# Optimization experiments

Hardware: AMD Instinct MI355X
Metric: run time of the kernel (lower is better)

## Reference

```python
import jax, jax.numpy as jnp
import numpy as np


def sage_pool(feat_src, edge_src, edge_dst, num_dst, W_pool, b_pool, W_self, W_neigh, bias):
    """DGL SAGEConv 'pool' aggregator on a bipartite block.
    feat_src: [N_src, in]; first num_dst rows are the dst nodes.
    """
    # per-src-node pool MLP, then gather per edge and scatter-max per dst
    m = jax.nn.relu(feat_src @ W_pool + b_pool)            # [N_src, in]
    agg = jax.ops.segment_max(m[edge_src], edge_dst, num_segments=num_dst)
    agg = jnp.where(jnp.isfinite(agg), agg, jnp.zeros((), agg.dtype))  # DGL: zero for 0-degree
    h_self = feat_src[:num_dst]
    return h_self @ W_self + agg @ W_neigh + bias          # [num_dst, out]


def setup_inputs() -> dict:
    key = jax.random.key(0)
    ks = jax.random.split(key, 16)
    F = 128                      # feat_dim_sum
    N0, N1, N2 = 409600, 40960, 4096
    E0, E1 = 409600, 40960
    inp = {
        "h_item": jax.random.normal(ks[0], (N0, F), jnp.float32),
        "h_item_dst": jax.random.normal(ks[1], (N2, F), jnp.float32),
        "edge_src0": jax.random.randint(ks[2], (E0,), 0, N0),
        "edge_dst0": jax.random.randint(ks[3], (E0,), 0, N1),
        "edge_src1": jax.random.randint(ks[4], (E1,), 0, N1),
        "edge_dst1": jax.random.randint(ks[5], (E1,), 0, N2),
        "num_mid": N1,
    }
    def lin(k, fan_in, fan_out):
        return jax.random.normal(k, (fan_in, fan_out), jnp.float32) / np.sqrt(fan_in)
    # layer 0: SAGEConv(128, 256, 'pool'); layer 1: SAGEConv(256, 128, 'pool')
    inp.update({
        "W_pool0": lin(ks[6], F, F),
        "b_pool0": jnp.zeros((F,), jnp.float32),
        "W_self0": lin(ks[7], F, 2 * F),
        "W_neigh0": lin(ks[8], F, 2 * F),
        "bias0": jnp.zeros((2 * F,), jnp.float32),
        "W_pool1": lin(ks[9], 2 * F, 2 * F),
        "b_pool1": jnp.zeros((2 * F,), jnp.float32),
        "W_self1": lin(ks[10], 2 * F, F),
        "W_neigh1": lin(ks[11], 2 * F, F),
        "bias1": jnp.zeros((F,), jnp.float32),
    })
    return inp


def reference(h_item, h_item_dst, edge_src0, edge_dst0, edge_src1, edge_dst1, num_mid,
              W_pool0, b_pool0, W_self0, W_neigh0, bias0,
              W_pool1, b_pool1, W_self1, W_neigh1, bias1):
    num_dst_final = h_item_dst.shape[0]
    h = sage_pool(h_item, edge_src0, edge_dst0, num_mid,
                  W_pool0, b_pool0, W_self0, W_neigh0, bias0)   # [N1, 2F]
    h = jax.nn.relu(h)  # dropout(0.2) is identity in eval mode
    h = sage_pool(h, edge_src1, edge_dst1, num_dst_final,
                  W_pool1, b_pool1, W_self1, W_neigh1, bias1)   # [N2, F]
    return h_item_dst + h
```

## Files before the change

### kernel.cpp

```cpp
#include <hip/hip_runtime.h>
#include <hip/hip_bf16.h>
#include <cstdint>


typedef unsigned int uint32;
typedef unsigned short ushort_t;

typedef __attribute__((ext_vector_type(8))) short short8v;
typedef __attribute__((ext_vector_type(4))) float float4v;

__device__ __forceinline__ float bf_to_f(unsigned short u) {
    union { uint32 u; float f; } cv; cv.u = ((uint32)u) << 16; return cv.f;
}
__device__ __forceinline__ unsigned short f_to_bf(float f) {
    union { float f; uint32 u; } cv; cv.f = f;
    uint32 u = cv.u;
    uint32 r = (u + 0x7FFFu + ((u >> 16) & 1u)) >> 16;
    return (unsigned short)r;
}

__device__ __forceinline__ int wave_incl_scan(int v) {
    #pragma unroll
    for (int s = 1; s < 64; s <<= 1) {
        int t = __shfl_up(v, s, 64);
        if ((int)(threadIdx.x & 63) >= s) v += t;
    }
    return v;
}

template<int KT, bool ABF>
__device__ __forceinline__ void gemm_seg(
    const void* __restrict__ Av, const ushort_t* __restrict__ Wp, int N,
    int row0, int col0, int tid, int wr, int wc, int l15, int g,
    ushort_t* lds, float4v (&acc)[4][4])
{
    constexpr int ldl = KT + 8;
    __syncthreads();
    if constexpr (ABF) {
        const ushort_t* A = (const ushort_t*)Av;
        constexpr int C8 = KT / 8;
        constexpr int TOT = 128 * C8;
        #pragma unroll 4
        for (int L = tid; L < TOT; L += 256) {
            int row = L / C8;
            int c8  = (L % C8) * 8;
            *(uint4*)&lds[row * ldl + c8] =
                *(const uint4*)(A + (size_t)(row0 + row) * KT + c8);
        }
    } else {
        const float* A = (const float*)Av;
        constexpr int C4 = KT / 4;
        constexpr int TOT = 128 * C4;
        #pragma unroll 4
        for (int L = tid; L < TOT; L += 256) {
            int row = L / C4;
            int c4  = (L % C4) * 4;
            float4 v = *(const float4*)(A + (size_t)(row0 + row) * KT + c4);
            ushort4 pk = make_ushort4(f_to_bf(v.x), f_to_bf(v.y), f_to_bf(v.z), f_to_bf(v.w));
            *(ushort4*)&lds[row * ldl + c4] = pk;
        }
    }
    __syncthreads();

    #pragma unroll
    for (int s = 0; s < KT / 32; ++s) {
        const int kb = s * 4 + g;
        short8v bfr[4], afr[4];
        #pragma unroll
        for (int ni = 0; ni < 4; ++ni) {
            int col = col0 + wc * 64 + ni * 16 + l15;
            bfr[ni] = *(const short8v*)(Wp + ((size_t)kb * N + col) * 8);
        }
        #pragma unroll
        for (int mi = 0; mi < 4; ++mi) {
            int row = wr * 64 + mi * 16 + l15;
            afr[mi] = *(const short8v*)&lds[row * ldl + s * 32 + g * 8];
        }
        #pragma unroll
        for (int mi = 0; mi < 4; ++mi)
            #pragma unroll
            for (int ni = 0; ni < 4; ++ni)
                acc[mi][ni] = __builtin_amdgcn_mfma_f32_16x16x32_bf16(
                    afr[mi], bfr[ni], acc[mi][ni], 0, 0, 0);
    }
}

template<bool RELU, bool BF16_OUT, bool HAS_ADD, int K0T, int K1T, bool A0BF, bool A1BF, int MINW>
__global__ __launch_bounds__(256, MINW) void gemm_mfma(
    const void* __restrict__ A0, const ushort_t* __restrict__ Wp0,
    const void* __restrict__ A1, const ushort_t* __restrict__ Wp1,
    const float* __restrict__ bias, const float* __restrict__ addsrc,
    void* __restrict__ Cout, int N)
{
    extern __shared__ ushort_t lds[];
    const int tid  = threadIdx.x;
    const int lane = tid & 63;
    const int wid  = tid >> 6;
    const int wr = wid >> 1, wc = wid & 1;
    const int row0 = blockIdx.x * 128;
    const int col0 = blockIdx.y * 128;
    const int l15 = lane & 15, g = lane >> 4;

    float4v acc[4][4];
    #pragma unroll
    for (int i = 0; i < 4; ++i)
        #pragma unroll
        for (int j = 0; j < 4; ++j)
            acc[i][j] = (float4v){0.f, 0.f, 0.f, 0.f};

    gemm_seg<K0T, A0BF>(A0, Wp0, N, row0, col0, tid, wr, wc, l15, g, lds, acc);
    if constexpr (K1T > 0)
        gemm_seg<K1T, A1BF>(A1, Wp1, N, row0, col0, tid, wr, wc, l15, g, lds, acc);

    if constexpr (BF16_OUT) {
        __syncthreads();
        #pragma unroll
        for (int mi = 0; mi < 4; ++mi) {
            #pragma unroll
            for (int ni = 0; ni < 4; ++ni) {
                const int rowl = wr * 64 + mi * 16 + g * 4;
                const int coll = wc * 64 + ni * 16 + l15;
                const float bs = bias[col0 + coll];
                #pragma unroll
                for (int q = 0; q < 4; ++q) {
                    float v = acc[mi][ni][q] + bs;
                    if (RELU) v = fmaxf(v, 0.f);
                    lds[(rowl + q) * 136 + coll] = f_to_bf(v);
                }
            }
        }
        __syncthreads();
        ushort_t* Cb = (ushort_t*)Cout;
        const int rloc = tid >> 4, c8 = (tid & 15) * 8;
        #pragma unroll
        for (int p = 0; p < 8; ++p) {
            int r = p * 16 + rloc;
            uint4 v = *(const uint4*)&lds[r * 136 + c8];
            *(uint4*)&Cb[(size_t)(row0 + r) * N + col0 + c8] = v;
        }
    } else {
        float* C = (float*)Cout;
        #pragma unroll
        for (int mi = 0; mi < 4; ++mi) {
            #pragma unroll
            for (int ni = 0; ni < 4; ++ni) {
                const int rowb = row0 + wr * 64 + mi * 16 + g * 4;
                const int col  = col0 + wc * 64 + ni * 16 + l15;
                const float bs = bias[col];
                #pragma unroll
                for (int q = 0; q < 4; ++q) {
                    float v = acc[mi][ni][q] + bs;
                    if (HAS_ADD) v += addsrc[(size_t)(rowb + q) * N + col];
                    if (RELU) v = fmaxf(v, 0.f);
                    C[(size_t)(rowb + q) * N + col] = v;
                }
            }
        }
    }
}

__global__ __launch_bounds__(256, 4) void pool0_fused(
    const float* __restrict__ hsrc, const ushort_t* __restrict__ Wp,
    const float* __restrict__ bias,
    const int* __restrict__ srcs, const int* __restrict__ dsts,
    int* __restrict__ agg, int E)
{
    constexpr int KT = 128, ldl = KT + 8;
    extern __shared__ ushort_t lds[];
    __shared__ int sIdx[128], sd[128];
    __shared__ int segbeg[129];
    __shared__ int wps[4];
    __shared__ int s_first_start, s_last_end;

    const int tid  = threadIdx.x;
    const int lane = tid & 63;
    const int wid  = tid >> 6;
    const int wr = wid >> 1, wc = wid & 1;
    const int l15 = lane & 15, g = lane >> 4;
    const int r0 = blockIdx.x * 128;

    if (tid < 128) { sIdx[tid] = srcs[r0 + tid]; sd[tid] = dsts[r0 + tid]; }
    __syncthreads();

    #pragma unroll 4
    for (int L = tid; L < 128 * 32; L += 256) {
        int row = L >> 5;
        int c4  = (L & 31) * 4;
        float4 v = *(const float4*)(hsrc + (size_t)sIdx[row] * KT + c4);
        ushort4 pk = make_ushort4(f_to_bf(v.x), f_to_bf(v.y), f_to_bf(v.z), f_to_bf(v.w));
        *(ushort4*)&lds[row * ldl + c4] = pk;
    }
    __syncthreads();

    float4v acc[4][4];
    #pragma unroll
    for (int i = 0; i < 4; ++i)
        #pragma unroll
        for (int j = 0; j < 4; ++j)
            acc[i][j] = (float4v){0.f, 0.f, 0.f, 0.f};

    #pragma unroll
    for (int s = 0; s < KT / 32; ++s) {
        const int kb = s * 4 + g;
        short8v bfr[4], afr[4];
        #pragma unroll
        for (int ni = 0; ni < 4; ++ni) {
            int col = wc * 64 + ni * 16 + l15;
            bfr[ni] = *(const short8v*)(Wp + ((size_t)kb * 128 + col) * 8);
        }
        #pragma unroll
        for (int mi = 0; mi < 4; ++mi) {
            int row = wr * 64 + mi * 16 + l15;
            afr[mi] = *(const short8v*)&lds[row * ldl + s * 32 + g * 8];
        }
        #pragma unroll
        for (int mi = 0; mi < 4; ++mi)
            #pragma unroll
            for (int ni = 0; ni < 4; ++ni)
                acc[mi][ni] = __builtin_amdgcn_mfma_f32_16x16x32_bf16(
                    afr[mi], bfr[ni], acc[mi][ni], 0, 0, 0);
    }

    __syncthreads();
    #pragma unroll
    for (int mi = 0; mi < 4; ++mi) {
        #pragma unroll
        for (int ni = 0; ni < 4; ++ni) {
            const int rowl = wr * 64 + mi * 16 + g * 4;
            const int coll = wc * 64 + ni * 16 + l15;
            const float bs = bias[coll];
            #pragma unroll
            for (int q = 0; q < 4; ++q) {
                float v = fmaxf(acc[mi][ni][q] + bs, 0.f);
                lds[(rowl + q) * ldl + coll] = f_to_bf(v);
            }
        }
    }

    int flag = 0;
    if (tid < 128) flag = (tid == 0) || (sd[tid] != sd[tid - 1]);
    int isc = wave_incl_scan(flag);
    if (lane == 63) wps[wid] = isc;
    if (tid == 0) {
        s_first_start = (r0 == 0) || (dsts[r0 - 1] != sd[0]);
        s_last_end    = (r0 + 128 == E) || (dsts[r0 + 128] != sd[127]);
    }
    __syncthreads();
    int woff = (wid >= 1) ? wps[0] : 0;
    if (tid < 128 && flag) segbeg[woff + isc - 1] = tid;
    __syncthreads();
    const int nseg = wps[0] + wps[1];
    const bool first_start = s_first_start, last_end = s_last_end;

    for (int it = tid; it < nseg * 64; it += 256) {
        int s  = it >> 6;
        int cp = it & 63;
        int beg = segbeg[s];
        int end = (s + 1 < nseg) ? segbeg[s + 1] : 128;
        int d = sd[beg];
        uint32 mx0 = 0, mx1 = 0;
        for (int r = beg; r < end; ++r) {
            ushort2 v = *(const ushort2*)&lds[r * ldl + cp * 2];
            if (v.x > mx0) mx0 = v.x;
            if (v.y > mx1) mx1 = v.y;
        }
        float f0 = bf_to_f((ushort_t)mx0), f1 = bf_to_f((ushort_t)mx1);
        int* p = agg + (size_t)d * 128 + cp * 2;
        bool interior = (s > 0 || first_start) && (s < nseg - 1 || last_end);
        if (interior) {
            *(float2*)p = make_float2(f0, f1);
        } else {
            atomicMax(p,     __float_as_int(f0));
            atomicMax(p + 1, __float_as_int(f1));
        }
    }
}

struct PSeg { const float* src; ushort_t* dst; int lgN; int N; int base; };

__global__ __launch_bounds__(256) void pack_weights(
    PSeg s0, PSeg s1, PSeg s2, PSeg s3, PSeg s4, PSeg s5, int total,
    int* __restrict__ cnt0, int n0, int* __restrict__ cnt1, int n1,
    float4* __restrict__ aggz, int nz4)
{
    int idx = blockIdx.x * 256 + threadIdx.x;
    int nth = gridDim.x * 256;
    if (idx < n0) cnt0[idx] = 0;
    if (idx < n1) cnt1[idx] = 0;
    for (int i = idx; i < nz4; i += nth)
        aggz[i] = make_float4(0.f, 0.f, 0.f, 0.f);
    if (idx >= total) return;
    PSeg s;
    if      (idx >= s5.base) s = s5;
    else if (idx >= s4.base) s = s4;
    else if (idx >= s3.base) s = s3;
    else if (idx >= s2.base) s = s2;
    else if (idx >= s1.base) s = s1;
    else                     s = s0;
    int e = idx - s.base;
    int k = e >> s.lgN;
    int n = e & (s.N - 1);
    s.dst[((size_t)(k >> 3) * s.N + n) * 8 + (k & 7)] = f_to_bf(s.src[e]);
}


__global__ __launch_bounds__(256) void count2_kernel(
    const int* __restrict__ edst0, int* __restrict__ cnt0, int E0,
    const int* __restrict__ edst1, int* __restrict__ cnt1, int E1)
{
    int e = blockIdx.x * 256 + threadIdx.x;
    if (e < E0) atomicAdd(&cnt0[edst0[e]], 1);
    int e1 = e - E0;
    if (e1 >= 0 && e1 < E1) atomicAdd(&cnt1[edst1[e1]], 1);
}

template<int C>
__device__ __forceinline__ void exscan_impl(
    const int* __restrict__ cnt, int* __restrict__ off, int* __restrict__ cur,
    int n, int* wsum)
{
    const int tid = threadIdx.x, lane = tid & 63, wid = tid >> 6;
    const int base = tid * C;
    int s = 0;
    #pragma unroll 4
    for (int i = 0; i < C; ++i) s += cnt[base + i];
    int is = wave_incl_scan(s);
    if (lane == 63) wsum[wid] = is;
    __syncthreads();
    if (wid == 0) {
        int w = (lane < 16) ? wsum[lane] : 0;
        int ws_ = wave_incl_scan(w);
        if (lane < 16) wsum[lane] = ws_ - w;
    }
    __syncthreads();
    int excl = wsum[wid] + is - s;
    #pragma unroll 4
    for (int i = 0; i < C; ++i) {
        int c = cnt[base + i];
        off[base + i] = excl;
        cur[base + i] = excl;
        excl += c;
    }
    if (tid == 1023) off[n] = excl;
}

__global__ __launch_bounds__(1024) void exscan2_kernel(
    const int* __restrict__ cnt0, int* __restrict__ off0, int* __restrict__ cur0, int n0,
    const int* __restrict__ cnt1, int* __restrict__ off1, int* __restrict__ cur1, int n1)
{
    __shared__ int wsum[16];
    if (blockIdx.x == 0) exscan_impl<40>(cnt0, off0, cur0, n0, wsum);
    else                 exscan_impl<4>(cnt1, off1, cur1, n1, wsum);
}

__global__ __launch_bounds__(256) void fill2_kernel(
    const int* __restrict__ esrc0, const int* __restrict__ edst0,
    int* __restrict__ cur0, int* __restrict__ srcs0, int* __restrict__ dsts0, int E0,
    const int* __restrict__ esrc1, const int* __restrict__ edst1,
    int* __restrict__ cur1, int* __restrict__ srcs1, int E1)
{
    int e = blockIdx.x * 256 + threadIdx.x;
    if (e < E0) {
        int d = edst0[e];
        int p = atomicAdd(&cur0[d], 1);
        srcs0[p] = esrc0[e];
        dsts0[p] = d;
    }
    int e1 = e - E0;
    if (e1 >= 0 && e1 < E1) {
        int p = atomicAdd(&cur1[edst1[e1]], 1);
        srcs1[p] = esrc1[e1];
    }
}

template<int F>
__global__ __launch_bounds__(256) void gather_max_kernel(
    const ushort_t* __restrict__ m, const int* __restrict__ off,
    const int* __restrict__ srcs, ushort_t* __restrict__ agg, int ndst)
{
    constexpr int PER = F / 64;
    int gw = (blockIdx.x * 256 + threadIdx.x) >> 6;
    if (gw >= ndst) return;
    int lane = threadIdx.x & 63;
    int beg = off[gw], end = off[gw + 1];
    ushort_t mx[PER];
    #pragma unroll
    for (int j = 0; j < PER; ++j) mx[j] = 0;
    for (int t = beg; t < end; ++t) {
        int s = srcs[t];
        const ushort_t* row = m + (size_t)s * F + lane * PER;
        ushort4 v = *(const ushort4*)row;
        mx[0] = mx[0] > v.x ? mx[0] : v.x;
        mx[1] = mx[1] > v.y ? mx[1] : v.y;
        mx[2] = mx[2] > v.z ? mx[2] : v.z;
        mx[3] = mx[3] > v.w ? mx[3] : v.w;
    }
    ushort_t* o = agg + (size_t)gw * F + lane * PER;
    *(ushort4*)o = make_ushort4(mx[0], mx[1], mx[2], mx[3]);
}


extern "C" void kernel_launch(void* const* d_in, const int* in_sizes, int n_in,
                              void* d_out, int out_size, void* d_ws, size_t ws_size,
                              hipStream_t stream)
{
    const float* h_item     = (const float*)d_in[0];
    const float* h_item_dst = (const float*)d_in[1];
    const int*   esrc0      = (const int*)d_in[2];
    const int*   edst0      = (const int*)d_in[3];
    const int*   esrc1      = (const int*)d_in[4];
    const int*   edst1      = (const int*)d_in[5];
    const float* W_pool0  = (const float*)d_in[7];
    const float* b_pool0  = (const float*)d_in[8];
    const float* W_self0  = (const float*)d_in[9];
    const float* W_neigh0 = (const float*)d_in[10];
    const float* bias0    = (const float*)d_in[11];
    const float* W_pool1  = (const float*)d_in[12];
    const float* b_pool1  = (const float*)d_in[13];
    const float* W_self1  = (const float*)d_in[14];
    const float* W_neigh1 = (const float*)d_in[15];
    const float* bias1    = (const float*)d_in[16];

    const int F  = 128;
    const int N0 = in_sizes[0] / F;
    const int N2 = in_sizes[1] / F;
    const int E0 = in_sizes[2];
    const int E1 = in_sizes[4];
    const int N1 = 40960;

    auto aup = [](size_t x) { return (x + 255) & ~(size_t)255; };
    char* p = (char*)d_ws;

    float* agg0 = (float*)p;           p += aup((size_t)N1 * F * 4);
    ushort_t* h = (ushort_t*)p;        p += aup((size_t)N1 * 2 * F * 2);
    ushort_t* m1 = (ushort_t*)p;       p += aup((size_t)N1 * 2 * F * 2);
    ushort_t* agg1 = (ushort_t*)p;     p += aup((size_t)N2 * 2 * F * 2);
    int* cnt0  = (int*)p;              p += aup((size_t)N1 * 4);
    int* off0  = (int*)p;              p += aup((size_t)(N1 + 1) * 4);
    int* cur0  = (int*)p;              p += aup((size_t)N1 * 4);
    int* srcs0 = (int*)p;              p += aup((size_t)E0 * 4);
    int* dsts0 = (int*)p;              p += aup((size_t)E0 * 4);
    int* cnt1  = (int*)p;              p += aup((size_t)N2 * 4);
    int* off1  = (int*)p;              p += aup((size_t)(N2 + 1) * 4);
    int* cur1  = (int*)p;              p += aup((size_t)N2 * 4);
    int* srcs1 = (int*)p;              p += aup((size_t)E1 * 4);
    ushort_t* wpk = (ushort_t*)p;      p += aup((size_t)212992 * 2);
    ushort_t* p_pool0  = wpk;
    ushort_t* p_self0  = p_pool0  + 128 * 128;
    ushort_t* p_neigh0 = p_self0  + 128 * 256;
    ushort_t* p_pool1  = p_neigh0 + 128 * 256;
    ushort_t* p_self1  = p_pool1  + 256 * 256;
    ushort_t* p_neigh1 = p_self1  + 256 * 128;

    {
        PSeg s0{W_pool0,  p_pool0,  7, 128, 0};
        PSeg s1{W_self0,  p_self0,  8, 256, 16384};
        PSeg s2{W_neigh0, p_neigh0, 8, 256, 49152};
        PSeg s3{W_pool1,  p_pool1,  8, 256, 81920};
        PSeg s4{W_self1,  p_self1,  7, 128, 147456};
        PSeg s5{W_neigh1, p_neigh1, 7, 128, 180224};
        const int total = 212992;
        pack_weights<<<(total + 255) / 256, 256, 0, stream>>>(
            s0, s1, s2, s3, s4, s5, total, cnt0, N1, cnt1, N2,
            (float4*)agg0, N1 * F / 4);
    }
    count2_kernel<<<(E0 + E1 + 255) / 256, 256, 0, stream>>>(
        edst0, cnt0, E0, edst1, cnt1, E1);
    exscan2_kernel<<<2, 1024, 0, stream>>>(cnt0, off0, cur0, N1, cnt1, off1, cur1, N2);
    fill2_kernel<<<(E0 + E1 + 255) / 256, 256, 0, stream>>>(
        esrc0, edst0, cur0, srcs0, dsts0, E0, esrc1, edst1, cur1, srcs1, E1);

    const uint32 LDS128 = (128 + 8) * 128 * 2;
    const uint32 LDS256 = (256 + 8) * 128 * 2;

    pool0_fused<<<E0 / 128, 256, LDS128, stream>>>(
        h_item, p_pool0, b_pool0, srcs0, dsts0, (int*)agg0, E0);

    {
        dim3 g(N1 / 128, (2 * F) / 128);
        gemm_mfma<true, true, false, 128, 128, false, false, 4><<<g, 256, LDS128, stream>>>(
            h_item, p_self0, agg0, p_neigh0, bias0, nullptr, (void*)h, 2 * F);
    }
    {
        dim3 g(N1 / 128, (2 * F) / 128);
        gemm_mfma<true, true, false, 256, 0, true, false, 2><<<g, 256, LDS256, stream>>>(
            h, p_pool1, nullptr, nullptr, b_pool1, nullptr, (void*)m1, 2 * F);
    }
    gather_max_kernel<256><<<(N2 + 3) / 4, 256, 0, stream>>>(m1, off1, srcs1, agg1, N2);

    {
        dim3 g(N2 / 128, F / 128);
        gemm_mfma<false, false, true, 256, 256, true, true, 2><<<g, 256, LDS256, stream>>>(
            h, p_self1, agg1, p_neigh1, bias1, h_item_dst, d_out, F);
    }
}
```

Before: 212.8 us.

## Fuse layer-1 pool GEMM with edge gather-max and merge prep into cooperative kernel

Layer 1 no longer computes the pool MLP for all 40960 mid nodes followed by a separate gather-max. A new pool1_fused kernel gathers source rows per edge (sorted by destination), runs the MFMA GEMM on those rows only, and does a segmented max into an fp32 agg1 buffer, using atomicMax only at tile boundaries. The four graph-prep kernels are merged into one cooperative kernel with grid.sync, with a multi-kernel fallback if the cooperative launch fails. This removes the m1 intermediate and several launches, at the cost of grid-sync overhead, a smaller single-block scan (256 threads instead of 1024), and the final GEMM now reading fp32 agg.

```diff
diff --git a/kernel.cpp b/kernel.cpp
--- a/kernel.cpp
+++ b/kernel.cpp
@@ -1,7 +1,10 @@
 #include <hip/hip_runtime.h>
 #include <hip/hip_bf16.h>
+#include <hip/hip_cooperative_groups.h>
 #include <cstdint>
 
+
+namespace cg = cooperative_groups;
 
 typedef unsigned int uint32;
 typedef unsigned short ushort_t;
@@ -276,20 +279,130 @@
     }
 }
 
+__global__ __launch_bounds__(256, 2) void pool1_fused(
+    const ushort_t* __restrict__ hsrc,
+    const ushort_t* __restrict__ Wp,
+    const float* __restrict__ bias,
+    const int* __restrict__ srcs, const int* __restrict__ dsts,
+    int* __restrict__ agg, int E)
+{
+    constexpr int KT = 256, ldl = KT + 8;
+    constexpr int ldt = 136;
+    extern __shared__ ushort_t lds[];
+    __shared__ int sIdx[128], sd[128];
+    __shared__ int segbeg[129];
+    __shared__ int wps[4];
+    __shared__ int s_first_start, s_last_end;
+
+    const int tid  = threadIdx.x;
+    const int lane = tid & 63;
+    const int wid  = tid >> 6;
+    const int wr = wid >> 1, wc = wid & 1;
+    const int l15 = lane & 15, g = lane >> 4;
+    const int r0 = blockIdx.x * 128;
+    const int col0 = blockIdx.y * 128;
+
+    if (tid < 128) { sIdx[tid] = srcs[r0 + tid]; sd[tid] = dsts[r0 + tid]; }
+    __syncthreads();
+
+    #pragma unroll 4
+    for (int L = tid; L < 128 * 32; L += 256) {
+        int row = L >> 5;
+        int c8  = (L & 31) * 8;
+        *(uint4*)&lds[row * ldl + c8] =
+            *(const uint4*)(hsrc + (size_t)sIdx[row] * KT + c8);
+    }
+    __syncthreads();
+
+    float4v acc[4][4];
+    #pragma unroll
+    for (int i = 0; i < 4; ++i)
+        #pragma unroll
+        for (int j = 0; j < 4; ++j)
+            acc[i][j] = (float4v){0.f, 0.f, 0.f, 0.f};
+
+    #pragma unroll
+    for (int s = 0; s < KT / 32; ++s) {
+        const int kb = s * 4 + g;
+        short8v bfr[4], afr[4];
+        #pragma unroll
+        for (int ni = 0; ni < 4; ++ni) {
+            int col = col0 + wc * 64 + ni * 16 + l15;
+            bfr[ni] = *(const short8v*)(Wp + ((size_t)kb * 256 + col) * 8);
+        }
+        #pragma unroll
+        for (int mi = 0; mi < 4; ++mi) {
+            int row = wr * 64 + mi * 16 + l15;
+            afr[mi] = *(const short8v*)&lds[row * ldl + s * 32 + g * 8];
+        }
+        #pragma unroll
+        for (int mi = 0; mi < 4; ++mi)
+            #pragma unroll
+            for (int ni = 0; ni < 4; ++ni)
+                acc[mi][ni] = __builtin_amdgcn_mfma_f32_16x16x32_bf16(
+                    afr[mi], bfr[ni], acc[mi][ni], 0, 0, 0);
+    }
+
+    __syncthreads();
+    #pragma unroll
+    for (int mi = 0; mi < 4; ++mi) {
+        #pragma unroll
+        for (int ni = 0; ni < 4; ++ni) {
+            const int rowl = wr * 64 + mi * 16 + g * 4;
+            const int coll = wc * 64 + ni * 16 + l15;
+            const float bs = bias[col0 + coll];
+            #pragma unroll
+            for (int q = 0; q < 4; ++q) {
+                float v = fmaxf(acc[mi][ni][q] + bs, 0.f);
+                lds[(rowl + q) * ldt + coll] = f_to_bf(v);
+            }
+        }
+    }
+
+    int flag = 0;
+    if (tid < 128) flag = (tid == 0) || (sd[tid] != sd[tid - 1]);
+    int isc = wave_incl_scan(flag);
+    if (lane == 63) wps[wid] = isc;
+    if (tid == 0) {
+        s_first_start = (r0 == 0) || (dsts[r0 - 1] != sd[0]);
+        s_last_end    = (r0 + 128 == E) || (dsts[r0 + 128] != sd[127]);
+    }
+    __syncthreads();
+    int woff = (wid >= 1) ? wps[0] : 0;
+    if (tid < 128 && flag) segbeg[woff + isc - 1] = tid;
+    __syncthreads();
+    const int nseg = wps[0] + wps[1];
+    const bool first_start = s_first_start, last_end = s_last_end;
+
+    for (int it = tid; it < nseg * 64; it += 256) {
+        int s  = it >> 6;
+        int cp = it & 63;
+        int beg = segbeg[s];
+        int end = (s + 1 < nseg) ? segbeg[s + 1] : 128;
+        int d = sd[beg];
+        uint32 mx0 = 0, mx1 = 0;
+        for (int r = beg; r < end; ++r) {
+            ushort2 v = *(const ushort2*)&lds[r * ldt + cp * 2];
+            if (v.x > mx0) mx0 = v.x;
+            if (v.y > mx1) mx1 = v.y;
+        }
+        float f0 = bf_to_f((ushort_t)mx0), f1 = bf_to_f((ushort_t)mx1);
+        int* p = agg + (size_t)d * 256 + col0 + cp * 2;
+        bool interior = (s > 0 || first_start) && (s < nseg - 1 || last_end);
+        if (interior) {
+            *(float2*)p = make_float2(f0, f1);
+        } else {
+            atomicMax(p,     __float_as_int(f0));
+            atomicMax(p + 1, __float_as_int(f1));
+        }
+    }
+}
+
 struct PSeg { const float* src; ushort_t* dst; int lgN; int N; int base; };
 
-__global__ __launch_bounds__(256) void pack_weights(
-    PSeg s0, PSeg s1, PSeg s2, PSeg s3, PSeg s4, PSeg s5, int total,
-    int* __restrict__ cnt0, int n0, int* __restrict__ cnt1, int n1,
-    float4* __restrict__ aggz, int nz4)
-{
-    int idx = blockIdx.x * 256 + threadIdx.x;
-    int nth = gridDim.x * 256;
-    if (idx < n0) cnt0[idx] = 0;
-    if (idx < n1) cnt1[idx] = 0;
-    for (int i = idx; i < nz4; i += nth)
-        aggz[i] = make_float4(0.f, 0.f, 0.f, 0.f);
-    if (idx >= total) return;
+__device__ __forceinline__ void pack_one(const PSeg& s0, const PSeg& s1,
+    const PSeg& s2, const PSeg& s3, const PSeg& s4, const PSeg& s5, int idx)
+{
     PSeg s;
     if      (idx >= s5.base) s = s5;
     else if (idx >= s4.base) s = s4;
@@ -303,100 +416,121 @@
     s.dst[((size_t)(k >> 3) * s.N + n) * 8 + (k & 7)] = f_to_bf(s.src[e]);
 }
 
-
-__global__ __launch_bounds__(256) void count2_kernel(
-    const int* __restrict__ edst0, int* __restrict__ cnt0, int E0,
-    const int* __restrict__ edst1, int* __restrict__ cnt1, int E1)
-{
-    int e = blockIdx.x * 256 + threadIdx.x;
-    if (e < E0) atomicAdd(&cnt0[edst0[e]], 1);
-    int e1 = e - E0;
-    if (e1 >= 0 && e1 < E1) atomicAdd(&cnt1[edst1[e1]], 1);
-}
-
-template<int C>
-__device__ __forceinline__ void exscan_impl(
-    const int* __restrict__ cnt, int* __restrict__ off, int* __restrict__ cur,
-    int n, int* wsum)
-{
+__device__ void exscan_b256(const int* __restrict__ cnt, int* __restrict__ off,
+                            int* __restrict__ cur, int n)
+{
+    __shared__ int wsum[4];
     const int tid = threadIdx.x, lane = tid & 63, wid = tid >> 6;
+    const int C = n >> 8;
     const int base = tid * C;
     int s = 0;
-    #pragma unroll 4
     for (int i = 0; i < C; ++i) s += cnt[base + i];
     int is = wave_incl_scan(s);
     if (lane == 63) wsum[wid] = is;
     __syncthreads();
-    if (wid == 0) {
-        int w = (lane < 16) ? wsum[lane] : 0;
-        int ws_ = wave_incl_scan(w);
-        if (lane < 16) wsum[lane] = ws_ - w;
+    if (tid == 0) {
+        int a = 0;
+        #pragma unroll
+        for (int j = 0; j < 4; ++j) { int t = wsum[j]; wsum[j] = a; a += t; }
     }
     __syncthreads();
     int excl = wsum[wid] + is - s;
-    #pragma unroll 4
     for (int i = 0; i < C; ++i) {
         int c = cnt[base + i];
         off[base + i] = excl;
         cur[base + i] = excl;
         excl += c;
     }
-    if (tid == 1023) off[n] = excl;
-}
-
-__global__ __launch_bounds__(1024) void exscan2_kernel(
-    const int* __restrict__ cnt0, int* __restrict__ off0, int* __restrict__ cur0, int n0,
-    const int* __restrict__ cnt1, int* __restrict__ off1, int* __restrict__ cur1, int n1)
-{
-    __shared__ int wsum[16];
-    if (blockIdx.x == 0) exscan_impl<40>(cnt0, off0, cur0, n0, wsum);
-    else                 exscan_impl<4>(cnt1, off1, cur1, n1, wsum);
-}
-
-__global__ __launch_bounds__(256) void fill2_kernel(
-    const int* __restrict__ esrc0, const int* __restrict__ edst0,
-    int* __restrict__ cur0, int* __restrict__ srcs0, int* __restrict__ dsts0, int E0,
-    const int* __restrict__ esrc1, const int* __restrict__ edst1,
-    int* __restrict__ cur1, int* __restrict__ srcs1, int E1)
-{
-    int e = blockIdx.x * 256 + threadIdx.x;
-    if (e < E0) {
-        int d = edst0[e];
-        int p = atomicAdd(&cur0[d], 1);
-        srcs0[p] = esrc0[e];
-        dsts0[p] = d;
-    }
-    int e1 = e - E0;
-    if (e1 >= 0 && e1 < E1) {
-        int p = atomicAdd(&cur1[edst1[e1]], 1);
-        srcs1[p] = esrc1[e1];
-    }
-}
-
-template<int F>
-__global__ __launch_bounds__(256) void gather_max_kernel(
-    const ushort_t* __restrict__ m, const int* __restrict__ off,
-    const int* __restrict__ srcs, ushort_t* __restrict__ agg, int ndst)
-{
-    constexpr int PER = F / 64;
-    int gw = (blockIdx.x * 256 + threadIdx.x) >> 6;
-    if (gw >= ndst) return;
-    int lane = threadIdx.x & 63;
-    int beg = off[gw], end = off[gw + 1];
-    ushort_t mx[PER];
-    #pragma unroll
-    for (int j = 0; j < PER; ++j) mx[j] = 0;
-    for (int t = beg; t < end; ++t) {
-        int s = srcs[t];
-        const ushort_t* row = m + (size_t)s * F + lane * PER;
-        ushort4 v = *(const ushort4*)row;
-        mx[0] = mx[0] > v.x ? mx[0] : v.x;
-        mx[1] = mx[1] > v.y ? mx[1] : v.y;
-        mx[2] = mx[2] > v.z ? mx[2] : v.z;
-        mx[3] = mx[3] > v.w ? mx[3] : v.w;
-    }
-    ushort_t* o = agg + (size_t)gw * F + lane * PER;
-    *(ushort4*)o = make_ushort4(mx[0], mx[1], mx[2], mx[3]);
+    if (tid == 255) off[n] = excl;
+}
+
+struct PrepArgs {
+    PSeg s0, s1, s2, s3, s4, s5; int wtotal;
+    const int *edst0, *esrc0; int E0;
+    const int *edst1, *esrc1; int E1;
+    int *cnt0, *off0, *cur0, *srcs0, *dsts0; int n0;
+    int *cnt1, *off1, *cur1, *srcs1, *dsts1; int n1;
+    float4 *agg0z; int nz0;
+    float4 *agg1z; int nz1;
+};
+
+__global__ __launch_bounds__(256) void prep_coop(PrepArgs a)
+{
+    cg::grid_group grid = cg::this_grid();
+    const int gid = blockIdx.x * 256 + threadIdx.x;
+    const int nth = gridDim.x * 256;
+    const float4 z4 = make_float4(0.f, 0.f, 0.f, 0.f);
+
+    for (int i = gid; i < a.n0; i += nth) a.cnt0[i] = 0;
+    for (int i = gid; i < a.n1; i += nth) a.cnt1[i] = 0;
+    for (int i = gid; i < a.nz0; i += nth) a.agg0z[i] = z4;
+    for (int i = gid; i < a.nz1; i += nth) a.agg1z[i] = z4;
+    for (int i = gid; i < a.wtotal; i += nth)
+        pack_one(a.s0, a.s1, a.s2, a.s3, a.s4, a.s5, i);
+    grid.sync();
+
+    for (int e = gid; e < a.E0; e += nth) atomicAdd(&a.cnt0[a.edst0[e]], 1);
+    for (int e = gid; e < a.E1; e += nth) atomicAdd(&a.cnt1[a.edst1[e]], 1);
+    grid.sync();
+
+    if (blockIdx.x == 0)      exscan_b256(a.cnt0, a.off0, a.cur0, a.n0);
+    else if (blockIdx.x == 1) exscan_b256(a.cnt1, a.off1, a.cur1, a.n1);
+    grid.sync();
+
+    for (int e = gid; e < a.E0; e += nth) {
+        int d = a.edst0[e];
+        int p = atomicAdd(&a.cur0[d], 1);
+        a.srcs0[p] = a.esrc0[e];
+        a.dsts0[p] = d;
+    }
+    for (int e = gid; e < a.E1; e += nth) {
+        int d = a.edst1[e];
+        int p = atomicAdd(&a.cur1[d], 1);
+        a.srcs1[p] = a.esrc1[e];
+        a.dsts1[p] = d;
+    }
+}
+
+__global__ __launch_bounds__(256) void prep_phase0(PrepArgs a)
+{
+    const int gid = blockIdx.x * 256 + threadIdx.x;
+    const int nth = gridDim.x * 256;
+    const float4 z4 = make_float4(0.f, 0.f, 0.f, 0.f);
+    for (int i = gid; i < a.n0; i += nth) a.cnt0[i] = 0;
+    for (int i = gid; i < a.n1; i += nth) a.cnt1[i] = 0;
+    for (int i = gid; i < a.nz0; i += nth) a.agg0z[i] = z4;
+    for (int i = gid; i < a.nz1; i += nth) a.agg1z[i] = z4;
+    for (int i = gid; i < a.wtotal; i += nth)
+        pack_one(a.s0, a.s1, a.s2, a.s3, a.s4, a.s5, i);
+}
+__global__ __launch_bounds__(256) void prep_count(PrepArgs a)
+{
+    const int gid = blockIdx.x * 256 + threadIdx.x;
+    const int nth = gridDim.x * 256;
+    for (int e = gid; e < a.E0; e += nth) atomicAdd(&a.cnt0[a.edst0[e]], 1);
+    for (int e = gid; e < a.E1; e += nth) atomicAdd(&a.cnt1[a.edst1[e]], 1);
+}
+__global__ __launch_bounds__(256) void prep_scan(PrepArgs a)
+{
+    if (blockIdx.x == 0)      exscan_b256(a.cnt0, a.off0, a.cur0, a.n0);
+    else if (blockIdx.x == 1) exscan_b256(a.cnt1, a.off1, a.cur1, a.n1);
+}
+__global__ __launch_bounds__(256) void prep_fill(PrepArgs a)
+{
+    const int gid = blockIdx.x * 256 + threadIdx.x;
+    const int nth = gridDim.x * 256;
+    for (int e = gid; e < a.E0; e += nth) {
+        int d = a.edst0[e];
+        int p = atomicAdd(&a.cur0[d], 1);
+        a.srcs0[p] = a.esrc0[e];
+        a.dsts0[p] = d;
+    }
+    for (int e = gid; e < a.E1; e += nth) {
+        int d = a.edst1[e];
+        int p = atomicAdd(&a.cur1[d], 1);
+        a.srcs1[p] = a.esrc1[e];
+        a.dsts1[p] = d;
+    }
 }
 
 
@@ -422,7 +556,6 @@
     const float* bias1    = (const float*)d_in[16];
 
     const int F  = 128;
-    const int N0 = in_sizes[0] / F;
     const int N2 = in_sizes[1] / F;
     const int E0 = in_sizes[2];
     const int E1 = in_sizes[4];
@@ -431,20 +564,20 @@
     auto aup = [](size_t x) { return (x + 255) & ~(size_t)255; };
     char* p = (char*)d_ws;
 
-    float* agg0 = (float*)p;           p += aup((size_t)N1 * F * 4);
-    ushort_t* h = (ushort_t*)p;        p += aup((size_t)N1 * 2 * F * 2);
-    ushort_t* m1 = (ushort_t*)p;       p += aup((size_t)N1 * 2 * F * 2);
-    ushort_t* agg1 = (ushort_t*)p;     p += aup((size_t)N2 * 2 * F * 2);
-    int* cnt0  = (int*)p;              p += aup((size_t)N1 * 4);
-    int* off0  = (int*)p;              p += aup((size_t)(N1 + 1) * 4);
-    int* cur0  = (int*)p;              p += aup((size_t)N1 * 4);
-    int* srcs0 = (int*)p;              p += aup((size_t)E0 * 4);
-    int* dsts0 = (int*)p;              p += aup((size_t)E0 * 4);
-    int* cnt1  = (int*)p;              p += aup((size_t)N2 * 4);
-    int* off1  = (int*)p;              p += aup((size_t)(N2 + 1) * 4);
-    int* cur1  = (int*)p;              p += aup((size_t)N2 * 4);
-    int* srcs1 = (int*)p;              p += aup((size_t)E1 * 4);
-    ushort_t* wpk = (ushort_t*)p;      p += aup((size_t)212992 * 2);
+    float* agg0 = (float*)p;        p += aup((size_t)N1 * F * 4);
+    ushort_t* h = (ushort_t*)p;     p += aup((size_t)N1 * 2 * F * 2);
+    float* agg1 = (float*)p;        p += aup((size_t)N2 * 2 * F * 4);
+    int* cnt0  = (int*)p;           p += aup((size_t)N1 * 4);
+    int* off0  = (int*)p;           p += aup((size_t)(N1 + 1) * 4);
+    int* cur0  = (int*)p;           p += aup((size_t)N1 * 4);
+    int* srcs0 = (int*)p;           p += aup((size_t)E0 * 4);
+    int* dsts0 = (int*)p;           p += aup((size_t)E0 * 4);
+    int* cnt1  = (int*)p;           p += aup((size_t)N2 * 4);
+    int* off1  = (int*)p;           p += aup((size_t)(N2 + 1) * 4);
+    int* cur1  = (int*)p;           p += aup((size_t)N2 * 4);
+    int* srcs1 = (int*)p;           p += aup((size_t)E1 * 4);
+    int* dsts1 = (int*)p;           p += aup((size_t)E1 * 4);
+    ushort_t* wpk = (ushort_t*)p;   p += aup((size_t)212992 * 2);
     ushort_t* p_pool0  = wpk;
     ushort_t* p_self0  = p_pool0  + 128 * 128;
     ushort_t* p_neigh0 = p_self0  + 128 * 256;
@@ -452,23 +585,33 @@
     ushort_t* p_self1  = p_pool1  + 256 * 256;
     ushort_t* p_neigh1 = p_self1  + 256 * 128;
 
+    PrepArgs pa;
+    pa.s0 = PSeg{W_pool0,  p_pool0,  7, 128, 0};
+    pa.s1 = PSeg{W_self0,  p_self0,  8, 256, 16384};
+    pa.s2 = PSeg{W_neigh0, p_neigh0, 8, 256, 49152};
+    pa.s3 = PSeg{W_pool1,  p_pool1,  8, 256, 81920};
+    pa.s4 = PSeg{W_self1,  p_self1,  7, 128, 147456};
+    pa.s5 = PSeg{W_neigh1, p_neigh1, 7, 128, 180224};
+    pa.wtotal = 212992;
+    pa.edst0 = edst0; pa.esrc0 = esrc0; pa.E0 = E0;
+    pa.edst1 = edst1; pa.esrc1 = esrc1; pa.E1 = E1;
+    pa.cnt0 = cnt0; pa.off0 = off0; pa.cur0 = cur0; pa.srcs0 = srcs0; pa.dsts0 = dsts0; pa.n0 = N1;
+    pa.cnt1 = cnt1; pa.off1 = off1; pa.cur1 = cur1; pa.srcs1 = srcs1; pa.dsts1 = dsts1; pa.n1 = N2;
+    pa.agg0z = (float4*)agg0; pa.nz0 = N1 * F / 4;
+    pa.agg1z = (float4*)agg1; pa.nz1 = N2 * 2 * F / 4;
+
     {
-        PSeg s0{W_pool0,  p_pool0,  7, 128, 0};
-        PSeg s1{W_self0,  p_self0,  8, 256, 16384};
-        PSeg s2{W_neigh0, p_neigh0, 8, 256, 49152};
-        PSeg s3{W_pool1,  p_pool1,  8, 256, 81920};
-        PSeg s4{W_self1,  p_self1,  7, 128, 147456};
-        PSeg s5{W_neigh1, p_neigh1, 7, 128, 180224};
-        const int total = 212992;
-        pack_weights<<<(total + 255) / 256, 256, 0, stream>>>(
-            s0, s1, s2, s3, s4, s5, total, cnt0, N1, cnt1, N2,
-            (float4*)agg0, N1 * F / 4);
-    }
-    count2_kernel<<<(E0 + E1 + 255) / 256, 256, 0, stream>>>(
-        edst0, cnt0, E0, edst1, cnt1, E1);
-    exscan2_kernel<<<2, 1024, 0, stream>>>(cnt0, off0, cur0, N1, cnt1, off1, cur1, N2);
-    fill2_kernel<<<(E0 + E1 + 255) / 256, 256, 0, stream>>>(
-        esrc0, edst0, cur0, srcs0, dsts0, E0, esrc1, edst1, cur1, srcs1, E1);
+        void* kargs[] = { (void*)&pa };
+        hipError_t ce = hipLaunchCooperativeKernel(
+            (const void*)prep_coop, dim3(1024), dim3(256), kargs, 0, stream);
+        if (ce != hipSuccess) {
+            (void)hipGetLastError();
+            prep_phase0<<<1024, 256, 0, stream>>>(pa);
+            prep_count <<<1024, 256, 0, stream>>>(pa);
+            prep_scan  <<<2,    256, 0, stream>>>(pa);
+            prep_fill  <<<1024, 256, 0, stream>>>(pa);
+        }
+    }
 
     const uint32 LDS128 = (128 + 8) * 128 * 2;
     const uint32 LDS256 = (256 + 8) * 128 * 2;
@@ -481,16 +624,16 @@
         gemm_mfma<true, true, false, 128, 128, false, false, 4><<<g, 256, LDS128, stream>>>(
             h_item, p_self0, agg0, p_neigh0, bias0, nullptr, (void*)h, 2 * F);
     }
+
     {
-        dim3 g(N1 / 128, (2 * F) / 128);
-        gemm_mfma<true, true, false, 256, 0, true, false, 2><<<g, 256, LDS256, stream>>>(
-            h, p_pool1, nullptr, nullptr, b_pool1, nullptr, (void*)m1, 2 * F);
-    }
-    gather_max_kernel<256><<<(N2 + 3) / 4, 256, 0, stream>>>(m1, off1, srcs1, agg1, N2);
+        dim3 g(E1 / 128, 2);
+        pool1_fused<<<g, 256, LDS256, stream>>>(
+            h, p_pool1, b_pool1, srcs1, dsts1, (int*)agg1, E1);
+    }
 
     {
         dim3 g(N2 / 128, F / 128);
-        gemm_mfma<false, false, true, 256, 256, true, true, 2><<<g, 256, LDS256, stream>>>(
+        gemm_mfma<false, false, true, 256, 256, true, false, 2><<<g, 256, LDS256, stream>>>(
             h, p_self1, agg1, p_neigh1, bias1, h_item_dst, d_out, F);
     }
 }
```

Result: slower. 620.7 us (+191.7%).
